# Kernel tuning notes

Measured on AMD Instinct MI355X. Metric: run time of the kernel, lower is better.

Reference implementation:

```python
import jax, jax.numpy as jnp
import numpy as np

# EKV constants from Config
VT = 0.025
N_FACTOR = 1.5
VD = 0.5
ALPHA = 2e-06
BASE_TIA = 500000.0

KERNEL = 3
STRIDE = 1
PAD = 1


def _unfold(x, k, stride, pad):
    # torch.nn.functional.unfold: (N, C, H, W) -> (N, C*k*k, L), patch dims ordered (c, kh, kw)
    N, C, H, W = x.shape
    xp = jnp.pad(x, ((0, 0), (0, 0), (pad, pad), (pad, pad)))
    Ho = (H + 2 * pad - k) // stride + 1
    Wo = (W + 2 * pad - k) // stride + 1
    patches = []
    for i in range(k):
        for j in range(k):
            patches.append(xp[:, :, i:i + stride * Ho:stride, j:j + stride * Wo:stride])
    # (k*k, N, C, Ho, Wo) -> (N, C, k*k, Ho*Wo) -> (N, C*k*k, L)
    p = jnp.stack(patches, axis=2)  # (N, C, k*k, Ho, Wo)
    return p.reshape(N, C * k * k, Ho * Wo), Ho, Wo


def setup_inputs() -> dict:
    key = jax.random.key(0)
    k1, k2 = jax.random.split(key)
    x = jax.random.normal(k1, (4, 64, 32, 32), dtype=jnp.float32)
    # theta ~ Normal(2.5, 0.5), shape (out_channels, in_channels, k, k)
    theta = 2.5 + 0.5 * jax.random.normal(k2, (64, 64, 3, 3), dtype=jnp.float32)
    return {"x": x, "theta": theta}


def reference(x, theta):
    N, C, H, W = x.shape
    O = theta.shape[0]
    fan_in = C * KERNEL * KERNEL
    tia_gain = BASE_TIA / (fan_in ** 0.5)
    phi = 2 * N_FACTOR * VT

    x_unf, Ho, Wo = _unfold(x, KERNEL, STRIDE, PAD)      # (N, C*k*k, L)
    x_in = x_unf[:, None, :, :]                           # (N, 1, CKK, L)
    w_th = theta.reshape(1, O, -1, 1)                     # (1, O, CKK, 1)

    v_diff = x_in - w_th                                  # (N, O, CKK, L)
    f_term = jnp.square(jax.nn.softplus(v_diff / phi))
    r_term = jnp.square(jax.nn.softplus((v_diff - VD) / phi))
    i_syn = ALPHA * (f_term - r_term)
    out_current = jnp.sum(i_syn, axis=2)                  # (N, O, L)
    out_voltage = out_current * tia_gain
    return out_voltage.reshape(N, O, Ho, Wo)
```

## Files before the change

kernel.cpp:

```cpp
#include <hip/hip_runtime.h>
#include <math.h>

#define HH 32
#define WW 32
#define CIN 64
#define NO 64
#define NCK 576
#define X_ELEMS 262144
#define STRIDE_E 292

#define WS_W    0
#define WS_TAU  36864

__device__ __forceinline__ float fexp2(float x) {
#if __has_builtin(__builtin_amdgcn_exp2f)
    return __builtin_amdgcn_exp2f(x);
#else
    return exp2f(x);
#endif
}
__device__ __forceinline__ float flog2(float x) {
#if __has_builtin(__builtin_amdgcn_logf)
    return __builtin_amdgcn_logf(x);
#else
    return log2f(x);
#endif
}

__global__ __launch_bounds__(256) void prep_kernel(const float* __restrict__ theta,
                                                   float* __restrict__ ws) {
    constexpr float SZ = 19.235933878519512f;
    const int b = blockIdx.x, t = threadIdx.x;
    if (b < 144) {
        int i = b * 256 + t;
        int o = i & 63, ck = i >> 6;
        float th = theta[o * NCK + ck];
        ws[WS_W + i] = -SZ * th;
        float mn = th;
#pragma unroll
        for (int s = 32; s > 0; s >>= 1)
            mn = fminf(mn, __shfl_xor(mn, s, 64));
        if (o == 0) ws[WS_TAU + ck] = SZ * mn - 8.0f;
    } else {
        if (t < 64) ws[WS_TAU + NCK + t] = 1e30f;
    }
}

__global__ __launch_bounds__(512) void ekv_kernel(
        const float* __restrict__ x, const float* __restrict__ ws,
        float* __restrict__ out) {
    constexpr float SZ = 19.235933878519512f;
    constexpr float C2 = 1.2726342e-3f;
    constexpr float OS = 0.020018875579925058f;

    __shared__ int   lc[8][STRIDE_E];
    __shared__ float lx[8][STRIDE_E];
    __shared__ float part[4][64];

    const int t    = threadIdx.x;
    const int lane = t & 63;
    const int wv   = __builtin_amdgcn_readfirstlane(t >> 6);
    const int p2   = (int)blockIdx.x * 8 + wv;
    const int pix  = p2 >> 1, half = p2 & 1;
    const int px   = wv >> 1;
    const int n  = pix >> 10;
    const int ho = (pix >> 5) & 31;
    const int wo = pix & 31;
    const int c0 = half * 32;

    int l = lane;
    int c_off = l / 9; if (c_off > 6) c_off = 6;
    int k = l - 9 * c_off; if (k > 8) k = 8;
    int di = k / 3, dj = k - 3 * (k / 3);
    int h = ho + di - 1, w_ = wo + dj - 1;
    bool sval = (h >= 0) && (h < HH) && (w_ >= 0) && (w_ < WW);
    int hc = min(max(h, 0), HH - 1), wc = min(max(w_, 0), WW - 1);
    float msc = ((l < 63) && sval) ? SZ : 0.0f;

    int gidx = n * (CIN * HH * WW) + (c0 + c_off) * 1024 + hc * WW + wc;
    const float* tw = ws + WS_TAU + c0 * 9;

    int cnt = 0;
    float xv = x[min(gidx, X_ELEMS - 1)];
    float tv = tw[l];

    for (int cb = 0; cb < 32; cb += 7) {
        int cc = 32 - cb; if (cc > 7) cc = 7;
        int gidx2 = gidx + 7 * 1024;
        const float* tw2 = tw + 63;
        float xvn = xv, tvn = tv;
        if (cb + 7 < 32) { xvn = x[min(gidx2, X_ELEMS - 1)]; tvn = tw2[l]; }

        float xs = xv * msc;
        bool a = (xs >= tv) && (l < cc * 9);
        unsigned long long act = __ballot(a);
        unsigned lo32 = (unsigned)act, hi32 = (unsigned)(act >> 32);
        int idx = __builtin_amdgcn_mbcnt_hi(hi32,
                      __builtin_amdgcn_mbcnt_lo(lo32, 0));
        if (a) {
            lc[wv][cnt + idx] = (c0 + cb) * 9 + l;
            lx[wv][cnt + idx] = xs;
        }
        cnt += (int)__popcll(act);
        gidx = gidx2; tw = tw2; xv = xvn; tv = tvn;
    }
    int padn = (-cnt) & 3;
    if (lane < padn) { lc[wv][cnt + lane] = 0; lx[wv][cnt + lane] = -100000.0f; }
    const int rounds = (cnt + padn) >> 2;

    const int4*   LC = (const int4*)&lc[wv][0];
    const float4* LX = (const float4*)&lx[wv][0];
    const float* wsW = ws + WS_W;

    float accF = 0.f, accR = 0.f;

#define EKV_BODY(SX, WV)                                                   \
    {                                                                      \
        float z  = (WV) + (SX);                        \
        float e  = fexp2(z);                                               \
        float f  = flog2(1.0f + e);                                        \
        float rr = flog2(fmaf(C2, e, 1.0f));                               \
        accF = fmaf(f, f, accF);                                           \
        accR = fmaf(rr, rr, accR);                                         \
    }

    if (rounds > 0) {
        int4   cq = LC[0];
        float4 xq = LX[0];
        for (int r = 0; r < rounds; ++r) {
            int4 cqn = cq; float4 xqn = xq;
            if (r + 1 < rounds) { cqn = LC[r + 1]; xqn = LX[r + 1]; }
            float W0 = wsW[(cq.x << 6) + lane];
            float W1 = wsW[(cq.y << 6) + lane];
            float W2 = wsW[(cq.z << 6) + lane];
            float W3 = wsW[(cq.w << 6) + lane];
            EKV_BODY(xq.x, W0)
            EKV_BODY(xq.y, W1)
            EKV_BODY(xq.z, W2)
            EKV_BODY(xq.w, W3)
            cq = cqn; xq = xqn;
        }
    }
#undef EKV_BODY

    float p = accF - accR;
    if (half == 1) part[px][lane] = p;
    __syncthreads();
    if (half == 0)
        out[((n * NO + lane) * HH + ho) * WW + wo] = (p + part[px][lane]) * OS;
}

extern "C" void kernel_launch(void* const* d_in, const int* in_sizes, int n_in,
                              void* d_out, int out_size, void* d_ws, size_t ws_size,
                              hipStream_t stream) {
    const float* x     = (const float*)d_in[0];
    const float* theta = (const float*)d_in[1];
    float* out = (float*)d_out;
    float* ws  = (float*)d_ws;

    prep_kernel<<<145, 256, 0, stream>>>(theta, ws);
    ekv_kernel <<<1024, 512, 0, stream>>>(x, ws, out);
}
```

Measured before the change: 72.46 us.

## Fuse prep into main kernel via cooperative launch with grid sync

Merges the theta preprocessing kernel into the main EKV kernel and launches it as a cooperative kernel with 512 blocks. A grid-wide sync separates preprocessing from compute, and each block now handles two pixel batches in a loop. This removes one kernel launch and its inter-kernel gap, at the cost of a grid barrier, halved grid parallelism, and the overhead of a cooperative launch.

```diff
diff --git a/kernel.cpp b/kernel.cpp
--- a/kernel.cpp
+++ b/kernel.cpp
@@ -1,5 +1,8 @@
 #include <hip/hip_runtime.h>
+#include <hip/hip_cooperative_groups.h>
 #include <math.h>
+
+namespace cg = cooperative_groups;
 
 #define HH 32
 #define WW 32
@@ -27,127 +30,132 @@
 #endif
 }
 
-__global__ __launch_bounds__(256) void prep_kernel(const float* __restrict__ theta,
-                                                   float* __restrict__ ws) {
-    constexpr float SZ = 19.235933878519512f;
-    const int b = blockIdx.x, t = threadIdx.x;
-    if (b < 144) {
-        int i = b * 256 + t;
-        int o = i & 63, ck = i >> 6;
-        float th = theta[o * NCK + ck];
-        ws[WS_W + i] = -SZ * th;
-        float mn = th;
-#pragma unroll
-        for (int s = 32; s > 0; s >>= 1)
-            mn = fminf(mn, __shfl_xor(mn, s, 64));
-        if (o == 0) ws[WS_TAU + ck] = SZ * mn - 8.0f;
-    } else {
-        if (t < 64) ws[WS_TAU + NCK + t] = 1e30f;
-    }
-}
-
 __global__ __launch_bounds__(512) void ekv_kernel(
-        const float* __restrict__ x, const float* __restrict__ ws,
-        float* __restrict__ out) {
+        const float* __restrict__ x, const float* __restrict__ theta,
+        float* __restrict__ ws, float* __restrict__ out) {
     constexpr float SZ = 19.235933878519512f;
     constexpr float C2 = 1.2726342e-3f;
     constexpr float OS = 0.020018875579925058f;
 
-    __shared__ int   lc[8][STRIDE_E];
-    __shared__ float lx[8][STRIDE_E];
+    __shared__ int   lcm[8][STRIDE_E];
+    __shared__ float lxm[8][STRIDE_E];
     __shared__ float part[4][64];
 
     const int t    = threadIdx.x;
+    const int b    = (int)blockIdx.x;
     const int lane = t & 63;
     const int wv   = __builtin_amdgcn_readfirstlane(t >> 6);
-    const int p2   = (int)blockIdx.x * 8 + wv;
-    const int pix  = p2 >> 1, half = p2 & 1;
-    const int px   = wv >> 1;
-    const int n  = pix >> 10;
-    const int ho = (pix >> 5) & 31;
-    const int wo = pix & 31;
-    const int c0 = half * 32;
 
-    int l = lane;
-    int c_off = l / 9; if (c_off > 6) c_off = 6;
-    int k = l - 9 * c_off; if (k > 8) k = 8;
-    int di = k / 3, dj = k - 3 * (k / 3);
-    int h = ho + di - 1, w_ = wo + dj - 1;
-    bool sval = (h >= 0) && (h < HH) && (w_ >= 0) && (w_ < WW);
-    int hc = min(max(h, 0), HH - 1), wc = min(max(w_, 0), WW - 1);
-    float msc = ((l < 63) && sval) ? SZ : 0.0f;
+    if (b < 144) {
+        if (t < 256) {
+            int i = b * 256 + t;
+            int o = i & 63, ck = i >> 6;
+            float th = theta[o * NCK + ck];
+            ws[WS_W + i] = -SZ * th;
+            float mn = th;
+#pragma unroll
+            for (int s = 32; s > 0; s >>= 1)
+                mn = fminf(mn, __shfl_xor(mn, s, 64));
+            if (o == 0) ws[WS_TAU + ck] = SZ * mn - 8.0f;
+        }
+    } else if (b == 144) {
+        if (t < 64) ws[WS_TAU + NCK + t] = 1e30f;
+    }
 
-    int gidx = n * (CIN * HH * WW) + (c0 + c_off) * 1024 + hc * WW + wc;
-    const float* tw = ws + WS_TAU + c0 * 9;
+    cg::this_grid().sync();
 
-    int cnt = 0;
-    float xv = x[min(gidx, X_ELEMS - 1)];
-    float tv = tw[l];
-
-    for (int cb = 0; cb < 32; cb += 7) {
-        int cc = 32 - cb; if (cc > 7) cc = 7;
-        int gidx2 = gidx + 7 * 1024;
-        const float* tw2 = tw + 63;
-        float xvn = xv, tvn = tv;
-        if (cb + 7 < 32) { xvn = x[min(gidx2, X_ELEMS - 1)]; tvn = tw2[l]; }
-
-        float xs = xv * msc;
-        bool a = (xs >= tv) && (l < cc * 9);
-        unsigned long long act = __ballot(a);
-        unsigned lo32 = (unsigned)act, hi32 = (unsigned)(act >> 32);
-        int idx = __builtin_amdgcn_mbcnt_hi(hi32,
-                      __builtin_amdgcn_mbcnt_lo(lo32, 0));
-        if (a) {
-            lc[wv][cnt + idx] = (c0 + cb) * 9 + l;
-            lx[wv][cnt + idx] = xs;
-        }
-        cnt += (int)__popcll(act);
-        gidx = gidx2; tw = tw2; xv = xvn; tv = tvn;
-    }
-    int padn = (-cnt) & 3;
-    if (lane < padn) { lc[wv][cnt + lane] = 0; lx[wv][cnt + lane] = -100000.0f; }
-    const int rounds = (cnt + padn) >> 2;
-
-    const int4*   LC = (const int4*)&lc[wv][0];
-    const float4* LX = (const float4*)&lx[wv][0];
     const float* wsW = ws + WS_W;
 
-    float accF = 0.f, accR = 0.f;
+    for (int pass = 0; pass < 2; ++pass) {
+        const int p2  = (b * 2 + pass) * 8 + wv;
+        const int pix = p2 >> 1, half = p2 & 1;
+        const int px  = wv >> 1;
+        const int n  = pix >> 10;
+        const int ho = (pix >> 5) & 31;
+        const int wo = pix & 31;
+        const int c0 = half * 32;
+
+        int l = lane;
+        int c_off = l / 9; if (c_off > 6) c_off = 6;
+        int k = l - 9 * c_off; if (k > 8) k = 8;
+        int di = k / 3, dj = k - 3 * (k / 3);
+        int h = ho + di - 1, w_ = wo + dj - 1;
+        bool sval = (h >= 0) && (h < HH) && (w_ >= 0) && (w_ < WW);
+        int hc = min(max(h, 0), HH - 1), wc = min(max(w_, 0), WW - 1);
+        float msc = ((l < 63) && sval) ? SZ : 0.0f;
+
+        int gidx = n * (CIN * HH * WW) + (c0 + c_off) * 1024 + hc * WW + wc;
+        const float* tw = ws + WS_TAU + c0 * 9;
+
+        int cnt = 0;
+        float xv = x[min(gidx, X_ELEMS - 1)];
+        float tv = tw[l];
+
+        for (int cb = 0; cb < 32; cb += 7) {
+            int cc = 32 - cb; if (cc > 7) cc = 7;
+            int gidx2 = gidx + 7 * 1024;
+            const float* tw2 = tw + 63;
+            float xvn = xv, tvn = tv;
+            if (cb + 7 < 32) { xvn = x[min(gidx2, X_ELEMS - 1)]; tvn = tw2[l]; }
+
+            float xs = xv * msc;
+            bool a = (xs >= tv) && (l < cc * 9);
+            unsigned long long act = __ballot(a);
+            unsigned lo32 = (unsigned)act, hi32 = (unsigned)(act >> 32);
+            int idx = __builtin_amdgcn_mbcnt_hi(hi32,
+                          __builtin_amdgcn_mbcnt_lo(lo32, 0));
+            if (a) {
+                lcm[wv][cnt + idx] = (c0 + cb) * 9 + l;
+                lxm[wv][cnt + idx] = xs;
+            }
+            cnt += (int)__popcll(act);
+            gidx = gidx2; tw = tw2; xv = xvn; tv = tvn;
+        }
+        int padn = (-cnt) & 3;
+        if (lane < padn) { lcm[wv][cnt + lane] = 0; lxm[wv][cnt + lane] = -100000.0f; }
+        const int rounds = (cnt + padn) >> 2;
+
+        const int4*   LC = (const int4*)&lcm[wv][0];
+        const float4* LX = (const float4*)&lxm[wv][0];
+
+        float accF = 0.f, accR = 0.f;
 
 #define EKV_BODY(SX, WV)                                                   \
-    {                                                                      \
-        float z  = (WV) + (SX);                        \
-        float e  = fexp2(z);                                               \
-        float f  = flog2(1.0f + e);                                        \
-        float rr = flog2(fmaf(C2, e, 1.0f));                               \
-        accF = fmaf(f, f, accF);                                           \
-        accR = fmaf(rr, rr, accR);                                         \
-    }
+        {                                                                  \
+            float z  = (WV) + (SX);                    \
+            float e  = fexp2(z);                                           \
+            float f  = flog2(1.0f + e);                                    \
+            float rr = flog2(fmaf(C2, e, 1.0f));                           \
+            accF = fmaf(f, f, accF);                                       \
+            accR = fmaf(rr, rr, accR);                                     \
+        }
 
-    if (rounds > 0) {
-        int4   cq = LC[0];
-        float4 xq = LX[0];
-        for (int r = 0; r < rounds; ++r) {
-            int4 cqn = cq; float4 xqn = xq;
-            if (r + 1 < rounds) { cqn = LC[r + 1]; xqn = LX[r + 1]; }
-            float W0 = wsW[(cq.x << 6) + lane];
-            float W1 = wsW[(cq.y << 6) + lane];
-            float W2 = wsW[(cq.z << 6) + lane];
-            float W3 = wsW[(cq.w << 6) + lane];
-            EKV_BODY(xq.x, W0)
-            EKV_BODY(xq.y, W1)
-            EKV_BODY(xq.z, W2)
-            EKV_BODY(xq.w, W3)
-            cq = cqn; xq = xqn;
+        if (rounds > 0) {
+            int4   cq = LC[0];
+            float4 xq = LX[0];
+            for (int r = 0; r < rounds; ++r) {
+                int4 cqn = cq; float4 xqn = xq;
+                if (r + 1 < rounds) { cqn = LC[r + 1]; xqn = LX[r + 1]; }
+                float W0 = wsW[(cq.x << 6) + lane];
+                float W1 = wsW[(cq.y << 6) + lane];
+                float W2 = wsW[(cq.z << 6) + lane];
+                float W3 = wsW[(cq.w << 6) + lane];
+                EKV_BODY(xq.x, W0)
+                EKV_BODY(xq.y, W1)
+                EKV_BODY(xq.z, W2)
+                EKV_BODY(xq.w, W3)
+                cq = cqn; xq = xqn;
+            }
         }
-    }
 #undef EKV_BODY
 
-    float p = accF - accR;
-    if (half == 1) part[px][lane] = p;
-    __syncthreads();
-    if (half == 0)
-        out[((n * NO + lane) * HH + ho) * WW + wo] = (p + part[px][lane]) * OS;
+        float p = accF - accR;
+        if (half == 1) part[px][lane] = p;
+        __syncthreads();
+        if (half == 0)
+            out[((n * NO + lane) * HH + ho) * WW + wo] = (p + part[px][lane]) * OS;
+        __syncthreads();
+    }
 }
 
 extern "C" void kernel_launch(void* const* d_in, const int* in_sizes, int n_in,
@@ -158,6 +166,7 @@
     float* out = (float*)d_out;
     float* ws  = (float*)d_ws;
 
-    prep_kernel<<<145, 256, 0, stream>>>(theta, ws);
-    ekv_kernel <<<1024, 512, 0, stream>>>(x, ws, out);
+    void* args[] = {(void*)&x, (void*)&theta, (void*)&ws, (void*)&out};
+    hipLaunchCooperativeKernel((const void*)ekv_kernel,
+                               dim3(512), dim3(512), args, 0, stream);
 }
```

Result: slower. 121.1 us (+67.2%).
